# Optimization experiments

Measured on AMD Instinct MI355X. Metric: run time of the kernel, lower is better.

The kernel has to match this reference:

```python
import jax, jax.numpy as jnp
import numpy as np

K = 3; PAD = 1; CIN = 64; COUT = 64; B = 4; H = 128; W = 128


def setup_inputs() -> dict:
    key = jax.random.key(0)
    k1, k2, k3 = jax.random.split(key, 3)
    x = jax.random.normal(k1, (B, CIN, H, W), dtype=jnp.float32)
    # offset-predicting conv: [2*K*K, Cin, K, K]; small init -> sub-pixel offsets
    w_off = jax.random.normal(k2, (2 * K * K, CIN, K, K), dtype=jnp.float32) * 0.01
    b_off = jnp.zeros((2 * K * K,), dtype=jnp.float32)
    # deformable conv weight (bias=False): [Cout, Cin, K, K]
    w_def = jax.random.normal(k3, (COUT, CIN, K, K), dtype=jnp.float32) * 0.05
    return {"x": x, "w_off": w_off, "b_off": b_off, "w_def": w_def}


def _deform_conv(x, w_off, b_off, w_def):
    Bb, Cin, Hh, Ww = x.shape
    KK = K * K
    # 1) predict offsets with a regular 3x3 conv (stride 1, pad 1)
    off = jax.lax.conv_general_dilated(
        x, w_off, window_strides=(1, 1), padding=[(PAD, PAD), (PAD, PAD)],
        dimension_numbers=("NCHW", "OIHW", "NCHW"))
    off = off + b_off[None, :, None, None]          # [B, 2*KK, H, W]
    off = off.reshape(Bb, KK, 2, Hh, Ww)            # torchvision layout: (dy, dx) per tap
    dy, dx = off[:, :, 0], off[:, :, 1]             # [B, KK, H, W]

    # 2) sampling coordinates: p = p0 + p_k + offset
    ky = (jnp.arange(KK) // K).astype(x.dtype)
    kx = (jnp.arange(KK) % K).astype(x.dtype)
    hh = jnp.arange(Hh, dtype=x.dtype)
    ww = jnp.arange(Ww, dtype=x.dtype)
    py = hh[None, None, :, None] - PAD + ky[None, :, None, None] + dy   # [B,KK,H,W]
    px = ww[None, None, None, :] - PAD + kx[None, :, None, None] + dx

    # 3) bilinear sampling with zero padding outside the image
    y0f = jnp.floor(py); x0f = jnp.floor(px)
    fy = py - y0f; fx = px - x0f
    y0 = y0f.astype(jnp.int32); x0 = x0f.astype(jnp.int32)
    x_flat = x.reshape(Bb, Cin, Hh * Ww)

    def gather(yi, xi):
        valid = (yi >= 0) & (yi < Hh) & (xi >= 0) & (xi < Ww)
        idx = jnp.clip(yi, 0, Hh - 1) * Ww + jnp.clip(xi, 0, Ww - 1)     # [B,KK,H,W]
        g = jax.vmap(lambda xf, ix: xf[:, ix.reshape(-1)])(x_flat, idx)  # [B,Cin,KK*H*W]
        return g.reshape(Bb, Cin, KK, Hh, Ww) * valid[:, None].astype(x.dtype)

    sampled = (gather(y0, x0)         * ((1 - fy) * (1 - fx))[:, None]
             + gather(y0, x0 + 1)     * ((1 - fy) * fx)[:, None]
             + gather(y0 + 1, x0)     * (fy * (1 - fx))[:, None]
             + gather(y0 + 1, x0 + 1) * (fy * fx)[:, None])               # [B,Cin,KK,H,W]

    # 4) convolution accumulation over (Cin, kernel taps)
    return jnp.einsum('bckhw,ock->bohw', sampled, w_def.reshape(COUT, Cin, KK))


def reference(x, w_off, b_off, w_def):
    return _deform_conv(x, w_off, b_off, w_def)
```

## Files before the change

kernel.cpp:

```cpp
#include <hip/hip_runtime.h>
#include <hip/hip_fp16.h>

#define Bn   4
#define CINc 64
#define COUTc 64
#define Hn   128
#define Wn   128
#define HW   (Hn * Wn)
#define KKc  9
#define NOFF 18

#define GRP  1040
#define ROWB (16 * GRP)
#define WREG (5 * ROWB)

typedef short bf16x8 __attribute__((ext_vector_type(8)));
typedef float f32x4  __attribute__((ext_vector_type(4)));
typedef float f32x2  __attribute__((ext_vector_type(2)));

__device__ inline unsigned short f2bf(float f) {
    unsigned int u = __float_as_uint(f);
    return (unsigned short)((u + 0x7fffu + ((u >> 16) & 1u)) >> 16);
}

__device__ inline void dma16(const void* g, void* l) {
#if __has_builtin(__builtin_amdgcn_global_load_lds)
    __builtin_amdgcn_global_load_lds(
        (__attribute__((address_space(1))) void*)(g),
        (__attribute__((address_space(3))) void*)(l), 16, 0, 0);
#else
    *(uint4*)l = *(const uint4*)g;
#endif
}

__global__ __launch_bounds__(256) void prep_all(
        const float* __restrict__ x, unsigned short* __restrict__ xt,
        const float* __restrict__ w_off, const float* __restrict__ w_def,
        unsigned short* __restrict__ wkb_sw, unsigned short* __restrict__ wob_sw) {
    int gb = blockIdx.x;
    int t  = threadIdx.x;
    if (gb < 256) {
        __shared__ unsigned short s16[64][264];
        int b  = gb >> 6;
        int hp = gb & 63;
        int w64 = t & 15, cg = t >> 4;

        const float* xb = x + (size_t)b * CINc * HW + (size_t)hp * 256;
        #pragma unroll
        for (int cc = 0; cc < 4; ++cc) {
            int c = cg * 4 + cc;
            #pragma unroll
            for (int j = 0; j < 4; ++j) {
                int px = j * 64 + w64 * 4;
                float4 v = *(const float4*)(xb + (size_t)c * HW + px);
                s16[c][px]     = f2bf(v.x);
                s16[c][px + 1] = f2bf(v.y);
                s16[c][px + 2] = f2bf(v.z);
                s16[c][px + 3] = f2bf(v.w);
            }
        }
        __syncthreads();

        int cpair = t & 31, pxg = t >> 5;
        unsigned* xtp = (unsigned*)xt;
        size_t gbase = (size_t)b * HW + (size_t)hp * 256;
        #pragma unroll
        for (int i = 0; i < 16; ++i) {
            int px = pxg * 32 + i * 2;
            unsigned a  = *(const unsigned*)&s16[cpair * 2][px];
            unsigned bl = *(const unsigned*)&s16[cpair * 2 + 1][px];
            unsigned d0 = (a & 0xFFFFu) | (bl << 16);
            unsigned d1 = (a >> 16) | (bl & 0xFFFF0000u);
            xtp[(gbase + px) * 32 + cpair]     = d0;
            xtp[(gbase + px + 1) * 32 + cpair] = d1;
        }
        return;
    }
    int idx = (gb - 256) * 256 + t;
    if (idx < 36864) {
        int j = idx & 7, l = (idx >> 3) & 63, s = idx >> 9;
        int k = s >> 3, kc = (s >> 2) & 1, ot = s & 3;
        int l15 = l & 15, quad = l >> 4;
        int o = ot * 16 + l15, c = kc * 32 + quad * 8 + j;
        wkb_sw[idx] = f2bf(w_def[((size_t)o * 64 + c) * 9 + k]);
    }
    int i2 = idx - 36864;
    if (i2 >= 0 && i2 < 18432) {
        int j = i2 & 7, l = (i2 >> 3) & 63, s = i2 >> 9;
        int tt = s >> 2, kc = (s >> 1) & 1, mt = s & 1;
        int l15 = l & 15, quad = l >> 4;
        int m = mt * 16 + l15, c = kc * 32 + quad * 8 + j;
        unsigned short v = 0;
        if (m < NOFF) v = f2bf(w_off[((size_t)m * 64 + c) * 9 + tt]);
        wob_sw[i2] = v;
    }
}


#define BFBUILD(C, kc, BF, W0, W1, W2, W3)                                   \
    do {                                                                     \
        const unsigned* t0 = (const unsigned*)&(C)[(kc) * 4 + 0];            \
        const unsigned* t1 = (const unsigned*)&(C)[(kc) * 4 + 1];            \
        const unsigned* b0 = (const unsigned*)&(C)[(kc) * 4 + 2];            \
        const unsigned* b1 = (const unsigned*)&(C)[(kc) * 4 + 3];            \
        _Pragma("unroll")                                                    \
        for (int jd = 0; jd < 4; ++jd) {                                     \
            f32x2 t0p = {__uint_as_float(t0[jd] << 16),                      \
                         __uint_as_float(t0[jd] & 0xFFFF0000u)};             \
            f32x2 t1p = {__uint_as_float(t1[jd] << 16),                      \
                         __uint_as_float(t1[jd] & 0xFFFF0000u)};             \
            f32x2 b0p = {__uint_as_float(b0[jd] << 16),                      \
                         __uint_as_float(b0[jd] & 0xFFFF0000u)};             \
            f32x2 b1p = {__uint_as_float(b1[jd] << 16),                      \
                         __uint_as_float(b1[jd] & 0xFFFF0000u)};             \
            f32x2 vv = t0p * (W0) + t1p * (W1) + b0p * (W2) + b1p * (W3);    \
            unsigned pk;                                                     \
            asm("v_cvt_pk_bf16_f32 %0, %1, %2"                               \
                : "=v"(pk) : "v"(vv.x), "v"(vv.y));                          \
            (BF).u[jd] = pk;                                                 \
        }                                                                    \
    } while (0)

#define TAP(k)                                                               \
    do {                                                                     \
        const uint4* C = R[(k) & 1];                                         \
        union { unsigned u; __half2 hv; } c01, c23;                          \
        c01.u = pw01[(k)]; c23.u = pw23[(k)];                                \
        float W0 = __low2float(c01.hv), W1 = __high2float(c01.hv);           \
        float W2 = __low2float(c23.hv), W3 = __high2float(c23.hv);           \
        union { bf16x8 v; unsigned u[4]; } bfa, bfb;                         \
        BFBUILD(C, 0, bfa, W0, W1, W2, W3);                                  \
        BFBUILD(C, 1, bfb, W0, W1, W2, W3);                                  \
        _Pragma("unroll")                                                    \
        for (int ot = 0; ot < 4; ++ot) {                                     \
            bf16x8 af0 = s_wv[(((k) * 2 + 0) * 4 + ot) * 64 + lane];         \
            acc[ot] = __builtin_amdgcn_mfma_f32_16x16x32_bf16(               \
                af0, bfa.v, acc[ot], 0, 0, 0);                               \
            bf16x8 af1 = s_wv[(((k) * 2 + 1) * 4 + ot) * 64 + lane];         \
            acc[ot] = __builtin_amdgcn_mfma_f32_16x16x32_bf16(               \
                af1, bfb.v, acc[ot], 0, 0, 0);                               \
        }                                                                    \
    } while (0)

#define FETCH_G(kk, st)                                              \
    do {                                                             \
        unsigned ad_ = ad[kk];                                       \
        unsigned xc_ = ad_ >> 16;                                    \
        unsigned at_ = (((ad_ & 255u) << 7) + xc_) << 6;             \
        unsigned ab_ = ((((ad_ >> 8) & 255u) << 7) + xc_) << 6;      \
        R[st][0] = *(const uint4*)(xtb + at_ + co0);                 \
        R[st][1] = *(const uint4*)(xtb + at_ + 64 + co0);            \
        R[st][2] = *(const uint4*)(xtb + ab_ + co0);                 \
        R[st][3] = *(const uint4*)(xtb + ab_ + 64 + co0);            \
        R[st][4] = *(const uint4*)(xtb + at_ + co1);                 \
        R[st][5] = *(const uint4*)(xtb + at_ + 64 + co1);            \
        R[st][6] = *(const uint4*)(xtb + ab_ + co1);                 \
        R[st][7] = *(const uint4*)(xtb + ab_ + 64 + co1);            \
    } while (0)

#define FETCH_L(kk, st)                                              \
    do {                                                             \
        unsigned ad_ = ad[kk];                                       \
        int x0_ = (int)(ad_ >> 16);                                  \
        int x1_ = x0_ + 1;                                           \
        int rt_ = ((int)(ad_ & 255u) - h + 2) * ROWB;                \
        int rb_ = ((int)((ad_ >> 8) & 255u) - h + 2) * ROWB;         \
        int a0_ = (x0_ >> 3) * GRP + (x0_ & 7) * 128;                \
        int a1_ = (x1_ >> 3) * GRP + (x1_ & 7) * 128;                \
        int j0  = (quad ^ (x0_ & 7)) << 4;                           \
        int j1  = (quad ^ (x1_ & 7)) << 4;                           \
        int j0b = ((4 + quad) ^ (x0_ & 7)) << 4;                     \
        int j1b = ((4 + quad) ^ (x1_ & 7)) << 4;                     \
        R[st][0] = *(const uint4*)(s_mem + rt_ + a0_ + j0);          \
        R[st][1] = *(const uint4*)(s_mem + rt_ + a1_ + j1);          \
        R[st][2] = *(const uint4*)(s_mem + rb_ + a0_ + j0);          \
        R[st][3] = *(const uint4*)(s_mem + rb_ + a1_ + j1);          \
        R[st][4] = *(const uint4*)(s_mem + rt_ + a0_ + j0b);         \
        R[st][5] = *(const uint4*)(s_mem + rt_ + a1_ + j1b);         \
        R[st][6] = *(const uint4*)(s_mem + rb_ + a0_ + j0b);         \
        R[st][7] = *(const uint4*)(s_mem + rb_ + a1_ + j1b);         \
    } while (0)

__global__ __launch_bounds__(512, 2) void fused_deform_v22(
        const unsigned short* __restrict__ xt,
        const unsigned short* __restrict__ wob_sw,
        const unsigned short* __restrict__ wkb_sw,
        const float* __restrict__ b_off, float* __restrict__ out) {
    extern __shared__ char s_mem[];
    const bf16x8* s_wv = (const bf16x8*)(s_mem + WREG);

    int gid  = blockIdx.x;
    int xcd  = gid & 7;
    int j    = gid >> 3;
    int hh   = j & 15;
    int b    = j >> 4;
    int h    = xcd * 16 + hh;
    int tid  = threadIdx.x;
    int lane = tid & 63;
    int wave = __builtin_amdgcn_readfirstlane(tid >> 6);
    int l15  = lane & 15;
    int quad = lane >> 4;
    int p    = wave * 16 + l15;

    const unsigned short* xtb = xt + (size_t)b * HW * 64;

    int xl = lane >> 3;
    int sl = lane & 7;
    #pragma unroll
    for (int i = 0; i < 10; ++i) {
        int slot = i * 8 + wave;
        int r  = slot >> 4;
        int g  = slot & 15;
        int y  = min(max(h - 2 + r, 0), Hn - 1);
        int xx = g * 8 + xl;
        int jj = sl ^ (xx & 7);
        dma16(xtb + ((size_t)y * Wn + xx) * 64 + jj * 8,
              s_mem + (size_t)r * ROWB + (size_t)g * GRP);
    }
    #pragma unroll
    for (int i = 0; i < 5; ++i) {
        int seg = i * 8 + wave;
        if (seg < 36)
            dma16((const uint4*)wob_sw + seg * 64 + lane,
                  s_mem + WREG + (size_t)seg * 1024);
    }
    __syncthreads();

    f32x4 oa0 = (f32x4){0.f, 0.f, 0.f, 0.f};
    f32x4 oa1 = (f32x4){0.f, 0.f, 0.f, 0.f};
    #pragma unroll
    for (int t9 = 0; t9 < 9; ++t9) {
        int ty = t9 / 3, tx = t9 % 3;
        int y  = h - 1 + ty;
        int xg = p - 1 + tx;
        bool v = (y >= 0) && (y < Hn) && (xg >= 0) && (xg < Wn);
        unsigned m = v ? 0xFFFFFFFFu : 0u;
        int yc = min(max(y, 0), Hn - 1);
        int xc = min(max(xg, 0), Wn - 1);
        int r  = yc - h + 2;
        int base = r * ROWB + (xc >> 3) * GRP + (xc & 7) * 128;
        uint4 L0 = *(const uint4*)(s_mem + base + ((quad ^ (xc & 7)) << 4));
        uint4 L1 = *(const uint4*)(s_mem + base + (((4 + quad) ^ (xc & 7)) << 4));
        #pragma unroll
        for (int kc = 0; kc < 2; ++kc) {
            union { bf16x8 v; uint4 u; } bf;
            bf.u = kc ? L1 : L0;
            bf.u.x &= m; bf.u.y &= m; bf.u.z &= m; bf.u.w &= m;
            bf16x8 a0 = s_wv[((t9 * 2 + kc) * 2 + 0) * 64 + lane];
            bf16x8 a1 = s_wv[((t9 * 2 + kc) * 2 + 1) * 64 + lane];
            oa0 = __builtin_amdgcn_mfma_f32_16x16x32_bf16(a0, bf.v, oa0, 0, 0, 0);
            oa1 = __builtin_amdgcn_mfma_f32_16x16x32_bf16(a1, bf.v, oa1, 0, 0, 0);
        }
    }

    unsigned my_ad[3]  = {0, 0, 0};
    unsigned my_w01[3] = {0, 0, 0};
    unsigned my_w23[3] = {0, 0, 0};
    auto phase1 = [&](int k, float dy, float dx, int slot) {
        float py  = (float)(h - 1 + k / 3) + dy;
        float pxf = (float)(p - 1 + k % 3) + dx;
        float y0f = floorf(py), x0f = floorf(pxf);
        float fy = py - y0f, fx = pxf - x0f;
        int y0 = (int)y0f, x0 = (int)x0f;
        bool vy0 = (y0 >= 0) & (y0 < Hn);
        bool vy1 = (y0 + 1 >= 0) & (y0 + 1 < Hn);
        bool vx0 = (x0 >= 0) & (x0 < Wn);
        bool vx1 = (x0 + 1 >= 0) & (x0 + 1 < Wn);
        float wy0 = vy0 ? 1.f - fy : 0.f;
        float wy1 = vy1 ? fy : 0.f;
        float wx0 = vx0 ? 1.f - fx : 0.f;
        float wx1 = vx1 ? fx : 0.f;
        int xc = min(max(x0, 0), Wn - 2);
        bool sel0 = (min(max(x0, 0), Wn - 1) != xc);
        bool sel1 = ((min(max(x0 + 1, 0), Wn - 1) - xc) == 1);
        float Wa = (sel0 ? 0.f : wx0) + (sel1 ? 0.f : wx1);
        float Wb = (sel0 ? wx0 : 0.f) + (sel1 ? wx1 : 0.f);
        int yc0 = min(max(y0, 0), Hn - 1), yc1 = min(max(y0 + 1, 0), Hn - 1);
        union { __half2 hv; unsigned u; } c01, c23;
        c01.hv = __floats2half2_rn(wy0 * Wa, wy0 * Wb);
        c23.hv = __floats2half2_rn(wy1 * Wa, wy1 * Wb);
        my_ad[slot]  = (unsigned)yc0 | ((unsigned)yc1 << 8) | ((unsigned)xc << 16);
        my_w01[slot] = c01.u;
        my_w23[slot] = c23.u;
    };
    int kb = quad * 2;
    phase1(kb,     oa0[0] + b_off[4 * quad],     oa0[1] + b_off[4 * quad + 1], 0);
    phase1(kb + 1, oa0[2] + b_off[4 * quad + 2], oa0[3] + b_off[4 * quad + 3], 1);
    if (quad == 0)
        phase1(8, oa1[0] + b_off[16], oa1[1] + b_off[17], 2);
    __syncthreads();

    #pragma unroll
    for (int i = 0; i < 9; ++i) {
        int seg = i * 8 + wave;
        dma16((const uint4*)wkb_sw + (size_t)seg * 64 + lane,
              s_mem + WREG + (size_t)seg * 1024);
    }

    unsigned ad[KKc], pw01[KKc], pw23[KKc];
    #pragma unroll
    for (int k = 0; k < KKc; ++k) {
        int src  = (k < 8) ? ((k >> 1) * 16 + l15) : l15;
        int slot = (k < 8) ? (k & 1) : 2;
        ad[k]   = (unsigned)__shfl((int)my_ad[slot],  src, 64);
        pw01[k] = (unsigned)__shfl((int)my_w01[slot], src, 64);
        pw23[k] = (unsigned)__shfl((int)my_w23[slot], src, 64);
    }
    __syncthreads();

    bool oow = false;
    #pragma unroll
    for (int k = 0; k < KKc; ++k) {
        int r0 = (int)(ad[k] & 255u) - h + 2;
        int r1 = (int)((ad[k] >> 8) & 255u) - h + 2;
        oow |= ((unsigned)r0 > 4u) | ((unsigned)r1 > 4u);
    }
    bool use_global = __any(oow);

    f32x4 acc[4];
    #pragma unroll
    for (int ot = 0; ot < 4; ++ot) acc[ot] = (f32x4){0.f, 0.f, 0.f, 0.f};

    uint4 R[2][8];
    int co0 = quad * 8, co1 = 32 + quad * 8;

    if (__builtin_expect(use_global, 0)) {
        FETCH_G(0, 0);
        FETCH_G(1, 1); TAP(0);
        FETCH_G(2, 0); TAP(1);
        FETCH_G(3, 1); TAP(2);
        FETCH_G(4, 0); TAP(3);
        FETCH_G(5, 1); TAP(4);
        FETCH_G(6, 0); TAP(5);
        FETCH_G(7, 1); TAP(6);
        FETCH_G(8, 0); TAP(7);
        TAP(8);
    } else {
        FETCH_L(0, 0);
        FETCH_L(1, 1); TAP(0);
        FETCH_L(2, 0); TAP(1);
        FETCH_L(3, 1); TAP(2);
        FETCH_L(4, 0); TAP(3);
        FETCH_L(5, 1); TAP(4);
        FETCH_L(6, 0); TAP(5);
        FETCH_L(7, 1); TAP(6);
        FETCH_L(8, 0); TAP(7);
        TAP(8);
    }

    #pragma unroll
    for (int ot = 0; ot < 4; ++ot)
        #pragma unroll
        for (int rr = 0; rr < 4; ++rr) {
            int o = ot * 16 + quad * 4 + rr;
            out[(((size_t)b * COUTc + o) * Hn + h) * Wn + p] = acc[ot][rr];
        }
}

extern "C" void kernel_launch(void* const* d_in, const int* in_sizes, int n_in,
                              void* d_out, int out_size, void* d_ws, size_t ws_size,
                              hipStream_t stream) {
    const float* x     = (const float*)d_in[0];
    const float* w_off = (const float*)d_in[1];
    const float* b_off = (const float*)d_in[2];
    const float* w_def = (const float*)d_in[3];
    float* out = (float*)d_out;

    char* ws = (char*)d_ws;
    unsigned short* xt = (unsigned short*)ws;
    ws += (size_t)Bn * HW * CINc * sizeof(unsigned short);
    unsigned short* wkb_sw = (unsigned short*)ws;
    ws += 36864 * sizeof(unsigned short);
    unsigned short* wob_sw = (unsigned short*)ws;

    static bool attr_set = false;
    if (!attr_set) {
        (void)hipFuncSetAttribute((const void*)fused_deform_v22,
                                  hipFuncAttributeMaxDynamicSharedMemorySize,
                                  156928);
        attr_set = true;
    }

    prep_all<<<256 + 216, 256, 0, stream>>>(x, xt, w_off, w_def, wkb_sw, wob_sw);
    fused_deform_v22<<<Bn * Hn, 512, 156928, stream>>>(xt, wob_sw, wkb_sw, b_off, out);
}
```

Before: 97.41 us.

## Fuse x transpose/bf16 conversion into main kernel and drop xt buffer

Removes the separate prep pass that transposed x into a channel-last bf16 buffer in global memory. The main kernel now loads fp32 NCHW rows directly, converts pairs of channels with v_cvt_pk_bf16_f32, and writes them into the swizzled LDS layout. The rare global fallback path gathers fp32 values per channel and converts them on the fly. This saves a full write and re-read of the transposed tensor and one kernel's worth of work. In exchange, each block reads a 5-row fp32 halo, so the same rows are loaded redundantly by neighbouring blocks, and the fallback gather becomes much more scattered.

```diff
diff --git a/kernel.cpp b/kernel.cpp
--- a/kernel.cpp
+++ b/kernel.cpp
@@ -33,50 +33,10 @@
 #endif
 }
 
-__global__ __launch_bounds__(256) void prep_all(
-        const float* __restrict__ x, unsigned short* __restrict__ xt,
+__global__ __launch_bounds__(256) void prep_tables(
         const float* __restrict__ w_off, const float* __restrict__ w_def,
         unsigned short* __restrict__ wkb_sw, unsigned short* __restrict__ wob_sw) {
-    int gb = blockIdx.x;
-    int t  = threadIdx.x;
-    if (gb < 256) {
-        __shared__ unsigned short s16[64][264];
-        int b  = gb >> 6;
-        int hp = gb & 63;
-        int w64 = t & 15, cg = t >> 4;
-
-        const float* xb = x + (size_t)b * CINc * HW + (size_t)hp * 256;
-        #pragma unroll
-        for (int cc = 0; cc < 4; ++cc) {
-            int c = cg * 4 + cc;
-            #pragma unroll
-            for (int j = 0; j < 4; ++j) {
-                int px = j * 64 + w64 * 4;
-                float4 v = *(const float4*)(xb + (size_t)c * HW + px);
-                s16[c][px]     = f2bf(v.x);
-                s16[c][px + 1] = f2bf(v.y);
-                s16[c][px + 2] = f2bf(v.z);
-                s16[c][px + 3] = f2bf(v.w);
-            }
-        }
-        __syncthreads();
-
-        int cpair = t & 31, pxg = t >> 5;
-        unsigned* xtp = (unsigned*)xt;
-        size_t gbase = (size_t)b * HW + (size_t)hp * 256;
-        #pragma unroll
-        for (int i = 0; i < 16; ++i) {
-            int px = pxg * 32 + i * 2;
-            unsigned a  = *(const unsigned*)&s16[cpair * 2][px];
-            unsigned bl = *(const unsigned*)&s16[cpair * 2 + 1][px];
-            unsigned d0 = (a & 0xFFFFu) | (bl << 16);
-            unsigned d1 = (a >> 16) | (bl & 0xFFFF0000u);
-            xtp[(gbase + px) * 32 + cpair]     = d0;
-            xtp[(gbase + px + 1) * 32 + cpair] = d1;
-        }
-        return;
-    }
-    int idx = (gb - 256) * 256 + t;
+    int idx = blockIdx.x * 256 + threadIdx.x;
     if (idx < 36864) {
         int j = idx & 7, l = (idx >> 3) & 63, s = idx >> 9;
         int k = s >> 3, kc = (s >> 2) & 1, ot = s & 3;
@@ -142,20 +102,36 @@
         }                                                                    \
     } while (0)
 
-#define FETCH_G(kk, st)                                              \
+__device__ inline uint4 gx_chunk(const float* __restrict__ xb,
+                                 int c0, int y, int xx) {
+    uint4 r;
+    unsigned* ru = (unsigned*)&r;
+    #pragma unroll
+    for (int w = 0; w < 4; ++w) {
+        float lo = xb[(size_t)(c0 + 2 * w) * HW + y * Wn + xx];
+        float hi = xb[(size_t)(c0 + 2 * w + 1) * HW + y * Wn + xx];
+        unsigned d;
+        asm("v_cvt_pk_bf16_f32 %0, %1, %2" : "=v"(d) : "v"(lo), "v"(hi));
+        ru[w] = d;
+    }
+    return r;
+}
+
+#define FETCH_GX(kk, st)                                             \
     do {                                                             \
         unsigned ad_ = ad[kk];                                       \
-        unsigned xc_ = ad_ >> 16;                                    \
-        unsigned at_ = (((ad_ & 255u) << 7) + xc_) << 6;             \
-        unsigned ab_ = ((((ad_ >> 8) & 255u) << 7) + xc_) << 6;      \
-        R[st][0] = *(const uint4*)(xtb + at_ + co0);                 \
-        R[st][1] = *(const uint4*)(xtb + at_ + 64 + co0);            \
-        R[st][2] = *(const uint4*)(xtb + ab_ + co0);                 \
-        R[st][3] = *(const uint4*)(xtb + ab_ + 64 + co0);            \
-        R[st][4] = *(const uint4*)(xtb + at_ + co1);                 \
-        R[st][5] = *(const uint4*)(xtb + at_ + 64 + co1);            \
-        R[st][6] = *(const uint4*)(xtb + ab_ + co1);                 \
-        R[st][7] = *(const uint4*)(xtb + ab_ + 64 + co1);            \
+        int xc_ = (int)(ad_ >> 16);                                  \
+        int yt_ = (int)(ad_ & 255u);                                 \
+        int yb_ = (int)((ad_ >> 8) & 255u);                          \
+        int c0_ = quad * 8, c1_ = 32 + quad * 8;                     \
+        R[st][0] = gx_chunk(xb4, c0_, yt_, xc_);                     \
+        R[st][1] = gx_chunk(xb4, c0_, yt_, xc_ + 1);                 \
+        R[st][2] = gx_chunk(xb4, c0_, yb_, xc_);                     \
+        R[st][3] = gx_chunk(xb4, c0_, yb_, xc_ + 1);                 \
+        R[st][4] = gx_chunk(xb4, c1_, yt_, xc_);                     \
+        R[st][5] = gx_chunk(xb4, c1_, yt_, xc_ + 1);                 \
+        R[st][6] = gx_chunk(xb4, c1_, yb_, xc_);                     \
+        R[st][7] = gx_chunk(xb4, c1_, yb_, xc_ + 1);                 \
     } while (0)
 
 #define FETCH_L(kk, st)                                              \
@@ -181,8 +157,8 @@
         R[st][7] = *(const uint4*)(s_mem + rb_ + a1_ + j1b);         \
     } while (0)
 
-__global__ __launch_bounds__(512, 2) void fused_deform_v22(
-        const unsigned short* __restrict__ xt,
+__global__ __launch_bounds__(512, 2) void fused_deform_v23(
+        const float* __restrict__ x,
         const unsigned short* __restrict__ wob_sw,
         const unsigned short* __restrict__ wkb_sw,
         const float* __restrict__ b_off, float* __restrict__ out) {
@@ -202,27 +178,39 @@
     int quad = lane >> 4;
     int p    = wave * 16 + l15;
 
-    const unsigned short* xtb = xt + (size_t)b * HW * 64;
-
-    int xl = lane >> 3;
-    int sl = lane & 7;
-    #pragma unroll
-    for (int i = 0; i < 10; ++i) {
-        int slot = i * 8 + wave;
-        int r  = slot >> 4;
-        int g  = slot & 15;
-        int y  = min(max(h - 2 + r, 0), Hn - 1);
-        int xx = g * 8 + xl;
-        int jj = sl ^ (xx & 7);
-        dma16(xtb + ((size_t)y * Wn + xx) * 64 + jj * 8,
-              s_mem + (size_t)r * ROWB + (size_t)g * GRP);
-    }
+    const float* xb4 = x + (size_t)b * CINc * HW;
+
     #pragma unroll
     for (int i = 0; i < 5; ++i) {
         int seg = i * 8 + wave;
         if (seg < 36)
             dma16((const uint4*)wob_sw + seg * 64 + lane,
                   s_mem + WREG + (size_t)seg * 1024);
+    }
+
+    #pragma unroll
+    for (int i = 0; i < 10; ++i) {
+        int T  = i * 512 + tid;
+        int f4 = T & 31;
+        int cp = (T >> 5) & 31;
+        int r  = T >> 10;
+        int y  = min(max(h - 2 + r, 0), Hn - 1);
+        const float* src = xb4 + (size_t)(2 * cp) * HW + y * Wn + f4 * 4;
+        float4 v0 = *(const float4*)src;
+        float4 v1 = *(const float4*)(src + HW);
+        const float* v0f = (const float*)&v0;
+        const float* v1f = (const float*)&v1;
+        int px0 = f4 * 4;
+        #pragma unroll
+        for (int e = 0; e < 4; ++e) {
+            int px = px0 + e;
+            unsigned d;
+            asm("v_cvt_pk_bf16_f32 %0, %1, %2"
+                : "=v"(d) : "v"(v0f[e]), "v"(v1f[e]));
+            int addr = r * ROWB + (px >> 3) * GRP + (px & 7) * 128
+                     + (((cp >> 2) ^ (px & 7)) << 4) + ((cp & 3) << 2);
+            *(unsigned*)(s_mem + addr) = d;
+        }
     }
     __syncthreads();
 
@@ -322,18 +310,17 @@
     for (int ot = 0; ot < 4; ++ot) acc[ot] = (f32x4){0.f, 0.f, 0.f, 0.f};
 
     uint4 R[2][8];
-    int co0 = quad * 8, co1 = 32 + quad * 8;
 
     if (__builtin_expect(use_global, 0)) {
-        FETCH_G(0, 0);
-        FETCH_G(1, 1); TAP(0);
-        FETCH_G(2, 0); TAP(1);
-        FETCH_G(3, 1); TAP(2);
-        FETCH_G(4, 0); TAP(3);
-        FETCH_G(5, 1); TAP(4);
-        FETCH_G(6, 0); TAP(5);
-        FETCH_G(7, 1); TAP(6);
-        FETCH_G(8, 0); TAP(7);
+        FETCH_GX(0, 0);
+        FETCH_GX(1, 1); TAP(0);
+        FETCH_GX(2, 0); TAP(1);
+        FETCH_GX(3, 1); TAP(2);
+        FETCH_GX(4, 0); TAP(3);
+        FETCH_GX(5, 1); TAP(4);
+        FETCH_GX(6, 0); TAP(5);
+        FETCH_GX(7, 1); TAP(6);
+        FETCH_GX(8, 0); TAP(7);
         TAP(8);
     } else {
         FETCH_L(0, 0);
@@ -367,20 +354,18 @@
     float* out = (float*)d_out;
 
     char* ws = (char*)d_ws;
-    unsigned short* xt = (unsigned short*)ws;
-    ws += (size_t)Bn * HW * CINc * sizeof(unsigned short);
     unsigned short* wkb_sw = (unsigned short*)ws;
     ws += 36864 * sizeof(unsigned short);
     unsigned short* wob_sw = (unsigned short*)ws;
 
     static bool attr_set = false;
     if (!attr_set) {
-        (void)hipFuncSetAttribute((const void*)fused_deform_v22,
+        (void)hipFuncSetAttribute((const void*)fused_deform_v23,
                                   hipFuncAttributeMaxDynamicSharedMemorySize,
                                   156928);
         attr_set = true;
     }
 
-    prep_all<<<256 + 216, 256, 0, stream>>>(x, xt, w_off, w_def, wkb_sw, wob_sw);
-    fused_deform_v22<<<Bn * Hn, 512, 156928, stream>>>(xt, wob_sw, wkb_sw, b_off, out);
-}
+    prep_tables<<<216, 256, 0, stream>>>(w_off, w_def, wkb_sw, wob_sw);
+    fused_deform_v23<<<Bn * Hn, 512, 156928, stream>>>(x, wob_sw, wkb_sw, b_off, out);
+}
```

After: 99.82 us. 1.02x slower.
